# Kernel tuning notes

Measured on AMD Instinct MI355X. Metric: run time of the kernel, lower is better.

## Reference

```python
import jax, jax.numpy as jnp
import numpy as np

N = 100000      # nodes
E = 800000      # directed edges (avg degree 8)
D_IN, D_HID, D_OUT = 512, 512, 256


def setup_inputs() -> dict:
    key = jax.random.key(0)
    ks = jax.random.split(key, 6)
    x = jax.random.normal(ks[0], (N, D_IN), dtype=jnp.float32)
    edge_index = jax.random.randint(ks[1], (2, E), 0, N, dtype=jnp.int32)
    W1 = jax.random.normal(ks[2], (D_IN, D_HID), dtype=jnp.float32) * (1.0 / np.sqrt(D_IN))
    b1 = jnp.zeros((D_HID,), dtype=jnp.float32)
    W2 = jax.random.normal(ks[3], (D_HID, D_OUT), dtype=jnp.float32) * (1.0 / np.sqrt(D_HID))
    b2 = jnp.zeros((D_OUT,), dtype=jnp.float32)
    return {"x": x, "edge_index": edge_index, "W1": W1, "b1": b1, "W2": W2, "b2": b2}


def gcn_conv(x, W, b, src, dst, n_nodes):
    # h = X W  (dense transform first, as in PyG GCNConv)
    h = x @ W                                              # [N, D_out]
    # symmetric normalization with self-loops already included in src/dst
    deg = jax.ops.segment_sum(jnp.ones(src.shape[0], dtype=h.dtype), dst,
                              num_segments=n_nodes)        # [N]
    dinv = jnp.where(deg > 0, jax.lax.rsqrt(deg), 0.0)
    norm = dinv[src] * dinv[dst]                           # [E+N]
    # gather -> scale -> scatter-add (message passing)
    msgs = h[src] * norm[:, None]                          # [E+N, D_out]
    out = jax.ops.segment_sum(msgs, dst, num_segments=n_nodes)
    return out + b


def reference(x, edge_index, W1, b1, W2, b2):
    n = x.shape[0]
    loops = jnp.arange(n, dtype=edge_index.dtype)          # add self-loops
    src = jnp.concatenate([edge_index[0], loops])
    dst = jnp.concatenate([edge_index[1], loops])
    h = jax.nn.relu(gcn_conv(x, W1, b1, src, dst, n))
    # F.dropout(training=False) is identity in eval mode
    h = gcn_conv(h, W2, b2, src, dst, n)
    return jax.nn.log_softmax(h, axis=1)
```

## Files before the change

### kernel.cpp

```cpp
#include <hip/hip_runtime.h>
#include <hip/hip_bf16.h>

#define NN   100000
#define NE   800000
#define DIN  512
#define DHID 512
#define DOUT 256
#define CAP  64

typedef short  s16x8 __attribute__((ext_vector_type(8)));
typedef float  f32x4 __attribute__((ext_vector_type(4)));

__device__ __forceinline__ float bf2f(unsigned short b) {
    union { unsigned u; float f; } c; c.u = ((unsigned)b) << 16; return c.f;
}
__device__ __forceinline__ unsigned short f2bf(float f) {
    union { float f; unsigned u; } c; c.f = f;
    unsigned u = c.u;
    u += 0x7FFFu + ((u >> 16) & 1u);
    return (unsigned short)(u >> 16);
}

__device__ __forceinline__ void gload_lds16(const void* g, void* l) {
    __builtin_amdgcn_global_load_lds(
        (const __attribute__((address_space(1))) void*)g,
        (__attribute__((address_space(3))) void*)l, 16, 0, 0);
}

__global__ void k_zero(int* cur) {
    int i = blockIdx.x * 256 + threadIdx.x;
    if (i < NN) cur[i] = 0;
}
__global__ void k_fill64(const int* __restrict__ src, const int* __restrict__ dst,
                         int* __restrict__ cur, int* __restrict__ col)
{
    int i = blockIdx.x * 256 + threadIdx.x;
    if (i < NE) {
        const int d = dst[i];
        const int slot = atomicAdd(&cur[d], 1);
        if (slot < CAP) col[(size_t)d * CAP + slot] = src[i];
    }
}
__global__ void k_dinv(const int* __restrict__ cur, float* __restrict__ dinv) {
    int i = blockIdx.x * 256 + threadIdx.x;
    if (i < NN) dinv[i] = rsqrtf((float)cur[i] + 1.0f);
}

__global__ __launch_bounds__(256) void k_x2bf(const float* __restrict__ x,
                                              unsigned short* __restrict__ xb)
{
    const size_t i = (size_t)(blockIdx.x * 256 + threadIdx.x) * 8;
    if (i >= (size_t)NN * DIN) return;
    const float4 v0 = *reinterpret_cast<const float4*>(x + i);
    const float4 v1 = *reinterpret_cast<const float4*>(x + i + 4);
    uint4 r;
    r.x = (unsigned)f2bf(v0.x) | ((unsigned)f2bf(v0.y) << 16);
    r.y = (unsigned)f2bf(v0.z) | ((unsigned)f2bf(v0.w) << 16);
    r.z = (unsigned)f2bf(v1.x) | ((unsigned)f2bf(v1.y) << 16);
    r.w = (unsigned)f2bf(v1.z) | ((unsigned)f2bf(v1.w) << 16);
    *reinterpret_cast<uint4*>(xb + i) = r;
}

__global__ __launch_bounds__(256) void k_wt_all(
    const float* __restrict__ W1, const float* __restrict__ W2,
    unsigned short* __restrict__ Wt1, unsigned short* __restrict__ Wt2)
{
    const int idx = blockIdx.x * 256 + threadIdx.x;
    if (idx < 512 * 512) {
        const int k = idx >> 9, n = idx & 511;
        Wt1[n * 512 + k] = f2bf(W1[idx]);
    } else {
        const int r = idx - 512 * 512;
        if (r < 512 * 256) {
            const int k = r >> 8, n = r & 255;
            Wt2[n * 512 + k] = f2bf(W2[r]);
        }
    }
}

template<int NC>
__global__ __launch_bounds__(256) void k_mfma_gemm(
    const unsigned short* __restrict__ A,
    const unsigned short* __restrict__ Wt,
    const float* __restrict__ dinv,
    unsigned short* __restrict__ Hb,
    int M)
{
    constexpr int K  = 512;
    constexpr int GN = NC / 128;
    __shared__ __align__(16) unsigned short As[128 * 32];
    __shared__ __align__(16) unsigned short Bs[128 * 32];

    const int GM  = (M + 127) >> 7;
    const int nwg = GM * GN;
    const int bid = blockIdx.x;
    const int q = nwg >> 3, r = nwg & 7;
    const int xcd = bid & 7, pos = bid >> 3;
    const int sbid = (xcd < r ? xcd * (q + 1) : r * (q + 1) + (xcd - r) * q) + pos;
    const int bm = (sbid / GN) * 128;
    const int bn = (sbid % GN) * 128;

    const int t    = threadIdx.x;
    const int lane = t & 63;
    const int wid  = t >> 6;
    const int wr = wid >> 1, wc = wid & 1;

    f32x4 acc[4][4];
    #pragma unroll
    for (int i = 0; i < 4; ++i)
        #pragma unroll
        for (int j = 0; j < 4; ++j)
            acc[i][j] = (f32x4){0.f, 0.f, 0.f, 0.f};

    const int r16 = lane & 15;
    const int kc  = lane >> 4;

    for (int k0 = 0; k0 < K; k0 += 32) {
        #pragma unroll
        for (int i = 0; i < 2; ++i) {
            const int c   = i * 256 + t;
            const int row = c >> 2;
            const int cp  = c & 3;
            const int sc  = cp ^ ((row >> 1) & 3);
            const int gr  = (bm + row < M) ? bm + row : M - 1;
            gload_lds16(A  + (size_t)gr * K + k0 + sc * 8,
                        &As[(size_t)(i * 256 + wid * 64) * 8]);
            gload_lds16(Wt + (size_t)(bn + row) * K + k0 + sc * 8,
                        &Bs[(size_t)(i * 256 + wid * 64) * 8]);
        }
        __syncthreads();

        s16x8 af[4], bf[4];
        #pragma unroll
        for (int i = 0; i < 4; ++i) {
            const int ra = wr * 64 + i * 16 + r16;
            af[i] = *reinterpret_cast<const s16x8*>(
                &As[ra * 32 + ((kc ^ ((ra >> 1) & 3)) * 8)]);
            const int rb = wc * 64 + i * 16 + r16;
            bf[i] = *reinterpret_cast<const s16x8*>(
                &Bs[rb * 32 + ((kc ^ ((rb >> 1) & 3)) * 8)]);
        }
        #pragma unroll
        for (int i = 0; i < 4; ++i)
            #pragma unroll
            for (int j = 0; j < 4; ++j)
                acc[i][j] = __builtin_amdgcn_mfma_f32_16x16x32_bf16(
                    af[i], bf[j], acc[i][j], 0, 0, 0);
        __syncthreads();
    }

    #pragma unroll
    for (int i = 0; i < 4; ++i) {
        #pragma unroll
        for (int r2 = 0; r2 < 4; ++r2) {
            const int m = bm + wr * 64 + i * 16 + (lane >> 4) * 4 + r2;
            if (m >= M) continue;
            const float s = dinv[m];
            #pragma unroll
            for (int j = 0; j < 4; ++j) {
                const int n = bn + wc * 64 + j * 16 + (lane & 15);
                Hb[(size_t)m * NC + n] = f2bf(acc[i][j][r2] * s);
            }
        }
    }
}

__device__ __forceinline__ void add8(const uint4 u, float* a) {
    a[0] += bf2f((unsigned short)(u.x));  a[1] += bf2f((unsigned short)(u.x >> 16));
    a[2] += bf2f((unsigned short)(u.y));  a[3] += bf2f((unsigned short)(u.y >> 16));
    a[4] += bf2f((unsigned short)(u.z));  a[5] += bf2f((unsigned short)(u.z >> 16));
    a[6] += bf2f((unsigned short)(u.w));  a[7] += bf2f((unsigned short)(u.w >> 16));
}

__global__ __launch_bounds__(256) void k_pull512(
    const int* __restrict__ cur, const int* __restrict__ col,
    const float* __restrict__ dinv, const unsigned short* __restrict__ H,
    const float* __restrict__ bias, unsigned short* __restrict__ Out)
{
    const int node = blockIdx.x * 4 + (threadIdx.x >> 6);
    if (node >= NN) return;
    const int lane = threadIdx.x & 63;

    float a[8] = {0.f, 0.f, 0.f, 0.f, 0.f, 0.f, 0.f, 0.f};
    add8(*reinterpret_cast<const uint4*>(H + (size_t)node * DHID + lane * 8), a);

    int deg = cur[node];
    if (deg > CAP) deg = CAP;
    const int* cl = col + (size_t)node * CAP;
    for (int e = 0; e < deg; ++e) {
        const int s = cl[e];
        add8(*reinterpret_cast<const uint4*>(H + (size_t)s * DHID + lane * 8), a);
    }

    const float sc = dinv[node];
    unsigned o[4];
    #pragma unroll
    for (int p = 0; p < 4; ++p) {
        float v0 = a[2 * p]     * sc + bias[lane * 8 + 2 * p];
        float v1 = a[2 * p + 1] * sc + bias[lane * 8 + 2 * p + 1];
        v0 = v0 > 0.f ? v0 : 0.f;
        v1 = v1 > 0.f ? v1 : 0.f;
        o[p] = (unsigned)f2bf(v0) | ((unsigned)f2bf(v1) << 16);
    }
    uint4 r = {o[0], o[1], o[2], o[3]};
    *reinterpret_cast<uint4*>(Out + (size_t)node * DHID + lane * 8) = r;
}

__device__ __forceinline__ void add4(const uint2 u, float* a) {
    a[0] += bf2f((unsigned short)(u.x));  a[1] += bf2f((unsigned short)(u.x >> 16));
    a[2] += bf2f((unsigned short)(u.y));  a[3] += bf2f((unsigned short)(u.y >> 16));
}

__global__ __launch_bounds__(256) void k_pull256_lsm(
    const int* __restrict__ cur, const int* __restrict__ col,
    const float* __restrict__ dinv, const unsigned short* __restrict__ H,
    const float* __restrict__ b2, float* __restrict__ out)
{
    const int node = blockIdx.x * 4 + (threadIdx.x >> 6);
    if (node >= NN) return;
    const int lane = threadIdx.x & 63;

    float a[4] = {0.f, 0.f, 0.f, 0.f};
    add4(*reinterpret_cast<const uint2*>(H + (size_t)node * DOUT + lane * 4), a);

    int deg = cur[node];
    if (deg > CAP) deg = CAP;
    const int* cl = col + (size_t)node * CAP;
    for (int e = 0; e < deg; ++e) {
        const int s = cl[e];
        add4(*reinterpret_cast<const uint2*>(H + (size_t)s * DOUT + lane * 4), a);
    }

    const float sc = dinv[node];
    float v0 = a[0] * sc + b2[lane * 4 + 0];
    float v1 = a[1] * sc + b2[lane * 4 + 1];
    float v2 = a[2] * sc + b2[lane * 4 + 2];
    float v3 = a[3] * sc + b2[lane * 4 + 3];

    float m = fmaxf(fmaxf(v0, v1), fmaxf(v2, v3));
    #pragma unroll
    for (int off = 32; off > 0; off >>= 1) m = fmaxf(m, __shfl_xor(m, off));
    float s = expf(v0 - m) + expf(v1 - m) + expf(v2 - m) + expf(v3 - m);
    #pragma unroll
    for (int off = 32; off > 0; off >>= 1) s += __shfl_xor(s, off);
    const float lse = m + logf(s);

    float4 rr = {v0 - lse, v1 - lse, v2 - lse, v3 - lse};
    *reinterpret_cast<float4*>(out + (size_t)node * DOUT + lane * 4) = rr;
}

extern "C" void kernel_launch(void* const* d_in, const int* in_sizes, int n_in,
                              void* d_out, int out_size, void* d_ws, size_t ws_size,
                              hipStream_t stream)
{
    const float* x  = (const float*)d_in[0];
    const int*   ei = (const int*)d_in[1];
    const float* W1 = (const float*)d_in[2];
    const float* b1 = (const float*)d_in[3];
    const float* W2 = (const float*)d_in[4];
    const float* b2 = (const float*)d_in[5];
    float* out = (float*)d_out;

    const int* src = ei;
    const int* dst = ei + NE;

    char* ws = (char*)d_ws;
    int*   cur  = (int*)(ws);
    float* dinv = (float*)(ws + (size_t)(1 << 19));
    int*   col  = (int*)(ws + (size_t)(1 << 20));
    unsigned short* Wt1 = (unsigned short*)(ws + (size_t)28 * (1 << 20));
    unsigned short* Wt2 = (unsigned short*)(ws + (size_t)29 * (1 << 20));
    unsigned short* P   = (unsigned short*)(ws + (size_t)32  * (1 << 20));
    unsigned short* Q   = (unsigned short*)(ws + (size_t)144 * (1 << 20));
    unsigned short* xb = P, * Hr = P;
    unsigned short* H1 = Q, * H2 = Q;

    const int g256n = (NN + 255) / 256;
    const int g256e = (NE + 255) / 256;

    k_zero  <<<g256n, 256, 0, stream>>>(cur);
    k_fill64<<<g256e, 256, 0, stream>>>(src, dst, cur, col);
    k_dinv  <<<g256n, 256, 0, stream>>>(cur, dinv);

    k_x2bf  <<<(int)(((size_t)NN * DIN / 8 + 255) / 256), 256, 0, stream>>>(x, xb);
    k_wt_all<<<(512 * 768 + 255) / 256, 256, 0, stream>>>(W1, W2, Wt1, Wt2);

    const int GM = (NN + 127) / 128;
    k_mfma_gemm<DHID><<<GM * (DHID / 128), 256, 0, stream>>>(xb, Wt1, dinv, H1, NN);
    k_pull512<<<(NN + 3) / 4, 256, 0, stream>>>(cur, col, dinv, H1, b1, Hr);

    k_mfma_gemm<DOUT><<<GM * (DOUT / 128), 256, 0, stream>>>(Hr, Wt2, dinv, H2, NN);
    k_pull256_lsm<<<(NN + 3) / 4, 256, 0, stream>>>(cur, col, dinv, H2, b2, out);
}
```

Measured before the change: 509.4 us.

## Fuse fp32-to-bf16 conversion of x into the first GEMM's A-operand loads

Drops the standalone x-to-bf16 kernel and adds a GEMM variant that reads fp32 x directly into registers, converting with packed bf16 conversion instructions before the MFMA. It removes the write and re-read of the intermediate bf16 copy of x. In exchange, A bypasses LDS and is loaded as fp32 by each of the four column-block workgroups, increasing global/L2 traffic and exposing load latency without double buffering.

```diff
diff --git a/kernel.cpp b/kernel.cpp
--- a/kernel.cpp
+++ b/kernel.cpp
@@ -20,6 +20,11 @@
     u += 0x7FFFu + ((u >> 16) & 1u);
     return (unsigned short)(u >> 16);
 }
+__device__ __forceinline__ unsigned cvtpk_bf16(float lo, float hi) {
+    unsigned r;
+    asm("v_cvt_pk_bf16_f32 %0, %1, %2" : "=v"(r) : "v"(lo), "v"(hi));
+    return r;
+}
 
 __device__ __forceinline__ void gload_lds16(const void* g, void* l) {
     __builtin_amdgcn_global_load_lds(
@@ -44,21 +49,6 @@
 __global__ void k_dinv(const int* __restrict__ cur, float* __restrict__ dinv) {
     int i = blockIdx.x * 256 + threadIdx.x;
     if (i < NN) dinv[i] = rsqrtf((float)cur[i] + 1.0f);
-}
-
-__global__ __launch_bounds__(256) void k_x2bf(const float* __restrict__ x,
-                                              unsigned short* __restrict__ xb)
-{
-    const size_t i = (size_t)(blockIdx.x * 256 + threadIdx.x) * 8;
-    if (i >= (size_t)NN * DIN) return;
-    const float4 v0 = *reinterpret_cast<const float4*>(x + i);
-    const float4 v1 = *reinterpret_cast<const float4*>(x + i + 4);
-    uint4 r;
-    r.x = (unsigned)f2bf(v0.x) | ((unsigned)f2bf(v0.y) << 16);
-    r.y = (unsigned)f2bf(v0.z) | ((unsigned)f2bf(v0.w) << 16);
-    r.z = (unsigned)f2bf(v1.x) | ((unsigned)f2bf(v1.y) << 16);
-    r.w = (unsigned)f2bf(v1.z) | ((unsigned)f2bf(v1.w) << 16);
-    *reinterpret_cast<uint4*>(xb + i) = r;
 }
 
 __global__ __launch_bounds__(256) void k_wt_all(
@@ -74,6 +64,106 @@
         if (r < 512 * 256) {
             const int k = r >> 8, n = r & 255;
             Wt2[n * 512 + k] = f2bf(W2[r]);
+        }
+    }
+}
+
+__global__ __launch_bounds__(256) void k_gemm1_ad(
+    const float* __restrict__ A,
+    const unsigned short* __restrict__ Wt,
+    const float* __restrict__ dinv,
+    unsigned short* __restrict__ Hb,
+    int M)
+{
+    constexpr int K = 512, NC = 512, GN = NC / 128;
+    __shared__ __align__(16) unsigned short Bs[128 * 32];
+
+    const int GM  = (M + 127) >> 7;
+    const int nwg = GM * GN;
+    const int bid = blockIdx.x;
+    const int q = nwg >> 3, r = nwg & 7;
+    const int xcd = bid & 7, pos = bid >> 3;
+    const int sbid = (xcd < r ? xcd * (q + 1) : r * (q + 1) + (xcd - r) * q) + pos;
+    const int bm = (sbid / GN) * 128;
+    const int bn = (sbid % GN) * 128;
+
+    const int t    = threadIdx.x;
+    const int lane = t & 63;
+    const int wid  = t >> 6;
+    const int wr = wid >> 1, wc = wid & 1;
+
+    f32x4 acc[4][4];
+    #pragma unroll
+    for (int i = 0; i < 4; ++i)
+        #pragma unroll
+        for (int j = 0; j < 4; ++j)
+            acc[i][j] = (f32x4){0.f, 0.f, 0.f, 0.f};
+
+    const int r16 = lane & 15;
+    const int kc  = lane >> 4;
+
+    const float* pa[4];
+    #pragma unroll
+    for (int i = 0; i < 4; ++i) {
+        int ar = bm + wr * 64 + i * 16 + r16;
+        if (ar >= M) ar = M - 1;
+        pa[i] = A + (size_t)ar * K + kc * 8;
+    }
+
+    for (int k0 = 0; k0 < K; k0 += 32) {
+        #pragma unroll
+        for (int i = 0; i < 2; ++i) {
+            const int c   = i * 256 + t;
+            const int row = c >> 2;
+            const int cp  = c & 3;
+            const int sc  = cp ^ ((row >> 1) & 3);
+            gload_lds16(Wt + (size_t)(bn + row) * K + k0 + sc * 8,
+                        &Bs[(size_t)(i * 256 + wid * 64) * 8]);
+        }
+
+        s16x8 af[4];
+        #pragma unroll
+        for (int i = 0; i < 4; ++i) {
+            const f32x4 lo = *reinterpret_cast<const f32x4*>(pa[i] + k0);
+            const f32x4 hi = *reinterpret_cast<const f32x4*>(pa[i] + k0 + 4);
+            uint4 p;
+            p.x = cvtpk_bf16(lo[0], lo[1]);
+            p.y = cvtpk_bf16(lo[2], lo[3]);
+            p.z = cvtpk_bf16(hi[0], hi[1]);
+            p.w = cvtpk_bf16(hi[2], hi[3]);
+            union { uint4 u; s16x8 s; } cv; cv.u = p;
+            af[i] = cv.s;
+        }
+        __syncthreads();
+
+        s16x8 bf[4];
+        #pragma unroll
+        for (int i = 0; i < 4; ++i) {
+            const int rb = wc * 64 + i * 16 + r16;
+            bf[i] = *reinterpret_cast<const s16x8*>(
+                &Bs[rb * 32 + ((kc ^ ((rb >> 1) & 3)) * 8)]);
+        }
+        #pragma unroll
+        for (int i = 0; i < 4; ++i)
+            #pragma unroll
+            for (int j = 0; j < 4; ++j)
+                acc[i][j] = __builtin_amdgcn_mfma_f32_16x16x32_bf16(
+                    af[i], bf[j], acc[i][j], 0, 0, 0);
+        __syncthreads();
+    }
+
+    #pragma unroll
+    for (int i = 0; i < 4; ++i) {
+        #pragma unroll
+        for (int r2 = 0; r2 < 4; ++r2) {
+            const int m = bm + wr * 64 + i * 16 + (lane >> 4) * 4 + r2;
+            if (m >= M) continue;
+            const float s = dinv[m];
+            #pragma unroll
+            for (int j = 0; j < 4; ++j) {
+                const int n = bn + wc * 64 + j * 16 + (lane & 15);
+                Hb[(size_t)m * NC + n] = f2bf(acc[i][j][r2] * s);
+            }
         }
     }
 }
@@ -270,9 +360,8 @@
     int*   col  = (int*)(ws + (size_t)(1 << 20));
     unsigned short* Wt1 = (unsigned short*)(ws + (size_t)28 * (1 << 20));
     unsigned short* Wt2 = (unsigned short*)(ws + (size_t)29 * (1 << 20));
-    unsigned short* P   = (unsigned short*)(ws + (size_t)32  * (1 << 20));
+    unsigned short* Hr  = (unsigned short*)(ws + (size_t)32  * (1 << 20));
     unsigned short* Q   = (unsigned short*)(ws + (size_t)144 * (1 << 20));
-    unsigned short* xb = P, * Hr = P;
     unsigned short* H1 = Q, * H2 = Q;
 
     const int g256n = (NN + 255) / 256;
@@ -281,12 +370,10 @@
     k_zero  <<<g256n, 256, 0, stream>>>(cur);
     k_fill64<<<g256e, 256, 0, stream>>>(src, dst, cur, col);
     k_dinv  <<<g256n, 256, 0, stream>>>(cur, dinv);
-
-    k_x2bf  <<<(int)(((size_t)NN * DIN / 8 + 255) / 256), 256, 0, stream>>>(x, xb);
     k_wt_all<<<(512 * 768 + 255) / 256, 256, 0, stream>>>(W1, W2, Wt1, Wt2);
 
     const int GM = (NN + 127) / 128;
-    k_mfma_gemm<DHID><<<GM * (DHID / 128), 256, 0, stream>>>(xb, Wt1, dinv, H1, NN);
+    k_gemm1_ad<<<GM * (DHID / 128), 256, 0, stream>>>(x, Wt1, dinv, H1, NN);
     k_pull512<<<(NN + 3) / 4, 256, 0, stream>>>(cur, col, dinv, H1, b1, Hr);
 
     k_mfma_gemm<DOUT><<<GM * (DOUT / 128), 256, 0, stream>>>(Hr, Wt2, dinv, H2, NN);
```

Result: slower. 605.0 us (+18.8%).
